# Optimization experiments

Hardware: AMD Instinct MI355X
Metric: run time of the kernel (lower is better)

Reference implementation:

```python
import jax, jax.numpy as jnp
import numpy as np
import math

NUM_HEADS = 8
Q_STRIDE = 2
KV_STRIDE = 2
POS_MAG = 1.0
WAVE_LEN = 1000.0


def _pos_embedding(h, w, h_kv, w_kv, feat_dim):
    # sinusoidal embedding of coordinate differences (in input-resolution units)
    h_idxs = jnp.arange(h, dtype=jnp.float32) * Q_STRIDE
    w_idxs = jnp.arange(w, dtype=jnp.float32) * Q_STRIDE
    h_kv_idxs = jnp.arange(h_kv, dtype=jnp.float32) * KV_STRIDE
    w_kv_idxs = jnp.arange(w_kv, dtype=jnp.float32) * KV_STRIDE
    h_diff = (h_idxs[:, None] - h_kv_idxs[None, :]) * POS_MAG  # [h, h_kv]
    w_diff = (w_idxs[:, None] - w_kv_idxs[None, :]) * POS_MAG  # [w, w_kv]
    feat_range = jnp.arange(feat_dim // 4, dtype=jnp.float32)
    dim_mat = WAVE_LEN ** (4.0 / feat_dim * feat_range)       # [feat_dim/4]
    ang_x = w_diff[:, :, None] / dim_mat                       # [w, w_kv, feat_dim/4]
    ang_y = h_diff[:, :, None] / dim_mat                       # [h, h_kv, feat_dim/4]
    emb_x = jnp.concatenate([jnp.sin(ang_x), jnp.cos(ang_x)], axis=2)  # [w, w_kv, feat_dim/2]
    emb_y = jnp.concatenate([jnp.sin(ang_y), jnp.cos(ang_y)], axis=2)  # [h, h_kv, feat_dim/2]
    return emb_x, emb_y


def setup_inputs() -> dict:
    key = jax.random.key(0)
    ks = jax.random.split(key, 10)
    n, C, H, W = 2, 256, 96, 96
    s = 0.05
    return {
        "x": jax.random.normal(ks[0], (n, C, H, W), jnp.float32),
        "Wq": jax.random.normal(ks[1], (C, C), jnp.float32) * s,
        "Wk": jax.random.normal(ks[2], (C, C), jnp.float32) * s,
        "Wv": jax.random.normal(ks[3], (C, C), jnp.float32) * s,
        "Wx": jax.random.normal(ks[4], (C, C // 2), jnp.float32) * s,
        "Wy": jax.random.normal(ks[5], (C, C // 2), jnp.float32) * s,
        "appr_bias": jax.random.normal(ks[6], (C,), jnp.float32) * s,
        "Wp": jax.random.normal(ks[7], (C, C), jnp.float32) * s,
        "bp": jax.random.normal(ks[8], (C,), jnp.float32) * s,
        "gamma": jax.random.normal(ks[9], (1,), jnp.float32),
    }


def reference(x, Wq, Wk, Wv, Wx, Wy, appr_bias, Wp, bp, gamma):
    n, C, H, W = x.shape
    g = NUM_HEADS
    d = C // g  # qk_embed_dim == v_dim
    # AvgPool2d(kernel_size=1, stride=s) == strided subsampling
    x_q = x[:, :, ::Q_STRIDE, ::Q_STRIDE]
    x_kv = x[:, :, ::KV_STRIDE, ::KV_STRIDE]
    h, w = x_q.shape[2], x_q.shape[3]
    h_kv, w_kv = x_kv.shape[2], x_kv.shape[3]

    # 1x1 convs (no bias) == channel matmuls
    q = jnp.einsum('oc,nchw->nohw', Wq, x_q)   # [n, C, h, w]
    k = jnp.einsum('oc,nchw->nohw', Wk, x_kv)  # [n, C, h_kv, w_kv]
    v = jnp.einsum('oc,nchw->nohw', Wv, x_kv)  # [n, C, h_kv, w_kv]

    emb_x, emb_y = _pos_embedding(h, w, h_kv, w_kv, C)
    inv_sqrt2 = 1.0 / math.sqrt(2.0)
    # Linear(feat_dim/2 -> C), split into heads, scale by 1/sqrt(2)
    pos_x = (jnp.einsum('wvf,of->wvo', emb_x, Wx).reshape(w, w_kv, g, d)
             .transpose(2, 0, 1, 3)) * inv_sqrt2  # [g, w, w_kv, d]
    pos_y = (jnp.einsum('huf,of->huo', emb_y, Wy).reshape(h, h_kv, g, d)
             .transpose(2, 0, 1, 3)) * inv_sqrt2  # [g, h, h_kv, d]

    qr = q.reshape(n, g, d, h, w).transpose(0, 1, 3, 4, 2)  # [n, g, h, w, d]
    kr = k.reshape(n, g, d, h_kv * w_kv)                     # [n, g, d, kv]

    # bias . key term, broadcast over query positions
    e_key = jnp.einsum('gd,ngdk->ngk', appr_bias.reshape(g, d), kr)
    e_key = e_key.reshape(n, g, 1, 1, h_kv, w_kv)
    # query . pos_x term (broadcast over h_kv), query . pos_y term (broadcast over w_kv)
    e_x = jnp.einsum('nghwd,gwvd->nghwv', qr, pos_x)[:, :, :, :, None, :]
    e_y = jnp.einsum('nghwd,ghud->nghwu', qr, pos_y)[:, :, :, :, :, None]

    energy = (e_key + e_x + e_y).reshape(n, g, h * w, h_kv * w_kv)
    attn = jax.nn.softmax(energy, axis=-1)  # [n, g, hw, kv]

    vr = v.reshape(n, g, d, h_kv * w_kv)  # [n, g, d, kv]
    out = jnp.einsum('ngqk,ngdk->ngdq', attn, vr).reshape(n, C, h, w)

    out = jnp.einsum('oc,nchw->nohw', Wp, out) + bp[None, :, None, None]
    out = jax.image.resize(out, (n, C, H, W), method='bilinear')
    return gamma * out + x
```

## Files before the change

kernel.cpp:

```cpp
#include <hip/hip_runtime.h>
#include <hip/hip_bf16.h>
#include <math.h>

#define NB 2
#define CC 256
#define NPOS 2304
#define NDELTA 95

typedef __attribute__((ext_vector_type(8))) short short8;
typedef __attribute__((ext_vector_type(4))) float floatx4;

__device__ inline unsigned short f2bf(float x) {
    unsigned int u = __float_as_uint(x);
    u = (u + 0x7FFFu + ((u >> 16) & 1u)) >> 16;
    return (unsigned short)u;
}
__device__ inline unsigned int pk2(float a, float b) {
    return (unsigned int)f2bf(a) | ((unsigned int)f2bf(b) << 16);
}
__device__ inline unsigned int pkmul(unsigned int a, unsigned int b) {
    __hip_bfloat162 x = *(__hip_bfloat162*)&a;
    __hip_bfloat162 y = *(__hip_bfloat162*)&b;
    __hip_bfloat162 r = __hmul2(x, y);
    return *(unsigned int*)&r;
}

__global__ __launch_bounds__(256) void pos_tables_kernel(
    const float* __restrict__ Wx, const float* __restrict__ Wy,
    const float* __restrict__ Wk, const float* __restrict__ ab,
    unsigned short* __restrict__ posxb, unsigned short* __restrict__ posyb,
    float* __restrict__ wkeff)
{
    int b = blockIdx.x;
    int t = threadIdx.x;
    if (b < NDELTA) {
        __shared__ float emb[128];
        float delta = (float)(b - 47);
        if (t < 64) {
            float dim_inv = exp2f(-(float)t * 0.15571537944784511f);
            float ang = 2.0f * delta * dim_inv;
            emb[t]      = sinf(ang);
            emb[t + 64] = cosf(ang);
        }
        __syncthreads();
        float sx = 0.f, sy = 0.f;
        const float* wxr = Wx + t * 128;
        const float* wyr = Wy + t * 128;
        for (int f = 0; f < 128; ++f) {
            float e = emb[f];
            sx += e * wxr[f];
            sy += e * wyr[f];
        }
        const float inv_sqrt2 = 0.70710678118654752440f;
        int g = t >> 5, d = t & 31;
        posxb[((size_t)g * 96 + b) * 32 + d] = f2bf(sx * inv_sqrt2);
        posyb[((size_t)g * 96 + b) * 32 + d] = f2bf(sy * inv_sqrt2);
    } else if (b < NDELTA + 8) {
        int g = b - NDELTA;
        float s = 0.f;
        for (int d = 0; d < 32; ++d)
            s += ab[g * 32 + d] * Wk[(g * 32 + d) * 256 + t];
        wkeff[g * 256 + t] = s;
    } else {
        int g = t >> 5, d = t & 31;
        posxb[((size_t)g * 96 + 95) * 32 + d] = 0;
        posyb[((size_t)g * 96 + 95) * 32 + d] = 0;
    }
}

__global__ __launch_bounds__(256) void extract_kernel(
    const float* __restrict__ x, float* __restrict__ xs)
{
    int idx = blockIdx.x * 256 + threadIdx.x;
    int f = idx * 4;
    int nc = f / NPOS;
    int rem = f - nc * NPOS;
    int i = rem / 48, j = rem - i * 48;
    const float* row = x + (size_t)nc * (96 * 96) + (2 * i) * 96 + 2 * j;
    *(float4*)(xs + f) = make_float4(row[0], row[2], row[4], row[6]);
}

__global__ __launch_bounds__(256) void wconv_kernel(
    const float* __restrict__ Wq, const float* __restrict__ Wv,
    const float* __restrict__ wkeff, const float* __restrict__ Wp,
    unsigned short* __restrict__ Wb, unsigned short* __restrict__ Wpb)
{
    int o = blockIdx.x;
    int t = threadIdx.x;
    if (o < 576) {
        float v = 0.f;
        if (o < 256)      v = Wq[o * 256 + t];
        else if (o < 512) v = Wv[(o - 256) * 256 + t];
        else if (o < 520) v = wkeff[(o - 512) * 256 + t];
        Wb[(size_t)o * 256 + t] = f2bf(v);
    } else {
        int o2 = o - 576;
        Wpb[(size_t)o2 * 256 + t] = f2bf(Wp[o2 * 256 + t]);
    }
}

__global__ __launch_bounds__(256) void qkv_kernel(
    const float* __restrict__ xs, const unsigned short* __restrict__ Wb,
    unsigned short* __restrict__ qbuf, float* __restrict__ vbuf,
    float* __restrict__ ek)
{
    __shared__ __align__(16) unsigned short Bt[64 * 40];
    int mTile = blockIdx.x;
    int nTile = blockIdx.y;
    int t = threadIdx.x;
    int m = t >> 6, L = t & 63, l16 = L & 15, oct = L >> 4;
    int colBase = nTile * 64;
    int n = colBase / NPOS;
    int p0 = colBase - n * NPOS;
    int o0 = mTile * 64 + m * 16;

    floatx4 acc[4] = {{0,0,0,0},{0,0,0,0},{0,0,0,0},{0,0,0,0}};

    int sc = t >> 4;
    int sp = (t & 15) * 4;
    for (int k0 = 0; k0 < 256; k0 += 32) {
        __syncthreads();
        #pragma unroll
        for (int i = 0; i < 2; ++i) {
            int c = k0 + i * 16 + sc;
            float4 v = *(const float4*)(xs + ((size_t)(n * 256 + c)) * NPOS + p0 + sp);
            int cl = i * 16 + sc;
            Bt[(sp + 0) * 40 + cl] = f2bf(v.x);
            Bt[(sp + 1) * 40 + cl] = f2bf(v.y);
            Bt[(sp + 2) * 40 + cl] = f2bf(v.z);
            Bt[(sp + 3) * 40 + cl] = f2bf(v.w);
        }
        short8 a = *(const short8*)(Wb + (size_t)(o0 + l16) * 256 + k0 + oct * 8);
        __syncthreads();
        #pragma unroll
        for (int f = 0; f < 4; ++f) {
            short8 b = *(const short8*)&Bt[(f * 16 + l16) * 40 + oct * 8];
            acc[f] = __builtin_amdgcn_mfma_f32_16x16x32_bf16(a, b, acc[f], 0, 0, 0);
        }
    }

    #pragma unroll
    for (int f = 0; f < 4; ++f) {
        int p = p0 + f * 16 + l16;
        #pragma unroll
        for (int r = 0; r < 4; ++r) {
            int o = o0 + oct * 4 + r;
            float val = acc[f][r];
            if (o < 256) {
                int g = o >> 5, d = o & 31;
                qbuf[((size_t)(n * 8 + g) * NPOS + p) * 32 + d] = f2bf(val);
            } else if (o < 512) {
                vbuf[((size_t)(n * 256 + (o - 256))) * NPOS + p] = val;
            } else if (o < 520) {
                ek[((size_t)(n * 8 + (o - 512))) * NPOS + p] = val;
            }
        }
    }
}

__global__ __launch_bounds__(256) void softA_kernel(float* __restrict__ ekA)
{
    int ng = blockIdx.x;
    float* e = ekA + (size_t)ng * NPOS;
    int t = threadIdx.x;
    __shared__ float red[256];
    float m = -1e30f;
    for (int k = t; k < NPOS; k += 256) m = fmaxf(m, e[k]);
    red[t] = m;
    __syncthreads();
    for (int s = 128; s > 0; s >>= 1) {
        if (t < s) red[t] = fmaxf(red[t], red[t + s]);
        __syncthreads();
    }
    m = red[0];
    for (int k = t; k < NPOS; k += 256) e[k] = __expf(e[k] - m);
}

__global__ __launch_bounds__(256) void vhat_kernel(
    const float* __restrict__ vbuf, const float* __restrict__ ekA,
    uint4* __restrict__ vhat)
{
    int tile = blockIdx.x;
    int ng = blockIdx.y;
    int k0 = tile * 96;
    int t = threadIdx.x;
    const float* vb = vbuf + (size_t)ng * 32 * NPOS;
    const float* Ab = ekA + (size_t)ng * NPOS;
    uint4* out = vhat + ((size_t)ng * 24 + tile) * 576;

    for (int s = t; s < 576; s += 256) {
        int grp = s >> 6;
        int Ls = s & 63;
        int cc = grp / 3;
        int nn = grp - cc * 3;
        int koct = cc * 32 + ((Ls >> 4) << 3);
        uint4 w = make_uint4(0u, 0u, 0u, 0u);
        if (nn < 2) {
            int d = nn * 16 + (Ls & 15);
            const float* vp = vb + (size_t)d * NPOS + k0 + koct;
            const float* ap = Ab + k0 + koct;
            float4 v0 = *(const float4*)vp;
            float4 v1 = *(const float4*)(vp + 4);
            float4 a0 = *(const float4*)ap;
            float4 a1 = *(const float4*)(ap + 4);
            w.x = pk2(v0.x * a0.x, v0.y * a0.y);
            w.y = pk2(v0.z * a0.z, v0.w * a0.w);
            w.z = pk2(v1.x * a1.x, v1.y * a1.y);
            w.w = pk2(v1.z * a1.z, v1.w * a1.w);
        } else if ((Ls & 15) == 0) {
            const float* ap = Ab + k0 + koct;
            float4 a0 = *(const float4*)ap;
            float4 a1 = *(const float4*)(ap + 4);
            w.x = pk2(a0.x, a0.y);
            w.y = pk2(a0.z, a0.w);
            w.z = pk2(a1.x, a1.y);
            w.w = pk2(a1.z, a1.w);
        }
        out[s] = w;
    }
}

#define DO_TILE(BB, TT) do {                                                   \
    int u0_ = (TT) * 2;                                                        \
    unsigned int y0_ = Ys[qp * 50 + u0_];     y0_ |= y0_ << 16;                \
    unsigned int y1_ = Ys[qp * 50 + u0_ + 1]; y1_ |= y1_ << 16;                \
    unsigned int Yc0_ = y0_, Yc1_ = (o < 2) ? y0_ : y1_, Yc2_ = y1_;           \
    union { unsigned int u[4]; short8 s; } av_;                                \
    av_.u[0] = pkmul(Xp[0], Yc0_); av_.u[1] = pkmul(Xp[1], Yc0_);              \
    av_.u[2] = pkmul(Xp[2], Yc0_); av_.u[3] = pkmul(Xp[3], Yc0_);              \
    acc0 = __builtin_amdgcn_mfma_f32_16x16x32_bf16(av_.s, *(const short8*)&BB[0], acc0, 0, 0, 0); \
    acc1 = __builtin_amdgcn_mfma_f32_16x16x32_bf16(av_.s, *(const short8*)&BB[1], acc1, 0, 0, 0); \
    acc2 = __builtin_amdgcn_mfma_f32_16x16x32_bf16(av_.s, *(const short8*)&BB[2], acc2, 0, 0, 0); \
    av_.u[0] = pkmul(Xp[4], Yc1_); av_.u[1] = pkmul(Xp[5], Yc1_);              \
    av_.u[2] = pkmul(Xp[6], Yc1_); av_.u[3] = pkmul(Xp[7], Yc1_);              \
    acc0 = __builtin_amdgcn_mfma_f32_16x16x32_bf16(av_.s, *(const short8*)&BB[3], acc0, 0, 0, 0); \
    acc1 = __builtin_amdgcn_mfma_f32_16x16x32_bf16(av_.s, *(const short8*)&BB[4], acc1, 0, 0, 0); \
    acc2 = __builtin_amdgcn_mfma_f32_16x16x32_bf16(av_.s, *(const short8*)&BB[5], acc2, 0, 0, 0); \
    av_.u[0] = pkmul(Xp[8], Yc2_); av_.u[1] = pkmul(Xp[9], Yc2_);              \
    av_.u[2] = pkmul(Xp[10], Yc2_); av_.u[3] = pkmul(Xp[11], Yc2_);            \
    acc0 = __builtin_amdgcn_mfma_f32_16x16x32_bf16(av_.s, *(const short8*)&BB[6], acc0, 0, 0, 0); \
    acc1 = __builtin_amdgcn_mfma_f32_16x16x32_bf16(av_.s, *(const short8*)&BB[7], acc1, 0, 0, 0); \
    acc2 = __builtin_amdgcn_mfma_f32_16x16x32_bf16(av_.s, *(const short8*)&BB[8], acc2, 0, 0, 0); \
} while (0)

__global__ __launch_bounds__(256, 2) void attn_kernel(
    const unsigned short* __restrict__ qbuf, const unsigned short* __restrict__ posxb,
    const unsigned short* __restrict__ posyb, const uint4* __restrict__ vhat,
    float* __restrict__ oattn)
{
    __shared__ unsigned short Xs[64 * 50];
    __shared__ unsigned short Ys[64 * 50];
    __shared__ float linv_s[64];

    int blk = blockIdx.x;
    int qt = blk % 36;
    int ng = blk / 36;
    int nb = ng >> 3, g = ng & 7;
    int qbase = qt * 64;
    int t = threadIdx.x;
    int m = t >> 6, L = t & 63;
    int l16 = L & 15, oct = L >> 4;

    {
        int qtile0 = qbase + m * 16;
        int hq = qtile0 / 48;
        int wq0 = qtile0 - hq * 48;
        short8 aq = *(const short8*)(qbuf +
            ((size_t)ng * NPOS + qtile0 + l16) * 32 + oct * 8);
        const unsigned short* pxg = posxb + (size_t)g * 96 * 32;
        const unsigned short* pyg = posyb + (size_t)g * 96 * 32;
        floatx4 zero = {0.f, 0.f, 0.f, 0.f};
        #pragma unroll
        for (int j = 0; j < 6; ++j) {
            int dl = j * 16 + l16;
            short8 bx = *(const short8*)(pxg + (size_t)dl * 32 + oct * 8);
            short8 by = *(const short8*)(pyg + (size_t)dl * 32 + oct * 8);
            floatx4 tx = __builtin_amdgcn_mfma_f32_16x16x32_bf16(aq, bx, zero, 0, 0, 0);
            floatx4 ty = __builtin_amdgcn_mfma_f32_16x16x32_bf16(aq, by, zero, 0, 0, 0);
            int u = hq + 47 - dl;
            bool uok = (u >= 0) && (u < 48);
            #pragma unroll
            for (int r = 0; r < 4; ++r) {
                int ql = oct * 4 + r;
                int v = wq0 + ql + 47 - dl;
                if (v >= 0 && v < 48)
                    Xs[(m * 16 + ql) * 50 + v] = f2bf(__expf(tx[r]));
                if (uok)
                    Ys[(m * 16 + ql) * 50 + u] = f2bf(__expf(ty[r]));
            }
        }
    }
    __syncthreads();

    int qp = m * 16 + l16;
    int o = oct;
    unsigned int Xp[12];
    #pragma unroll
    for (int c = 0; c < 3; ++c)
        #pragma unroll
        for (int jj = 0; jj < 4; ++jj) {
            int k = c * 32 + o * 8 + jj * 2;
            int v0 = (k < 48) ? k : k - 48;
            Xp[c * 4 + jj] = *(const unsigned int*)&Xs[qp * 50 + v0];
        }

    floatx4 acc0 = {0.f, 0.f, 0.f, 0.f};
    floatx4 acc1 = {0.f, 0.f, 0.f, 0.f};
    floatx4 acc2 = {0.f, 0.f, 0.f, 0.f};

    const uint4* vb = vhat + (size_t)ng * 24 * 576 + L;
    uint4 Abuf[9], Bbuf[9];
    #pragma unroll
    for (int gg = 0; gg < 9; ++gg) Abuf[gg] = vb[gg * 64];

    for (int tile = 0; tile < 24; tile += 2) {
        const uint4* sB = vb + (tile + 1) * 576;
        #pragma unroll
        for (int gg = 0; gg < 9; ++gg) Bbuf[gg] = sB[gg * 64];
        DO_TILE(Abuf, tile);
        if (tile + 2 < 24) {
            const uint4* sA = vb + (tile + 2) * 576;
            #pragma unroll
            for (int gg = 0; gg < 9; ++gg) Abuf[gg] = sA[gg * 64];
        }
        DO_TILE(Bbuf, tile + 1);
    }

    if ((L & 15) == 0) {
        int qc = m * 16 + (L >> 4) * 4;
        #pragma unroll
        for (int r = 0; r < 4; ++r)
            linv_s[qc + r] = 1.0f / acc2[r];
    }
    __syncthreads();
    {
        int qc = m * 16 + (L >> 4) * 4;
        float4 li = *(const float4*)&linv_s[qc];
        int d0 = L & 15;
        float* r0 = oattn + ((size_t)(nb * 256 + g * 32 + d0)) * NPOS + qbase + qc;
        *(float4*)r0 = make_float4(acc0[0] * li.x, acc0[1] * li.y,
                                   acc0[2] * li.z, acc0[3] * li.w);
        float* r1 = oattn + ((size_t)(nb * 256 + g * 32 + 16 + d0)) * NPOS + qbase + qc;
        *(float4*)r1 = make_float4(acc1[0] * li.x, acc1[1] * li.y,
                                   acc1[2] * li.z, acc1[3] * li.w);
    }
}

__global__ __launch_bounds__(256) void proj_kernel(
    const float* __restrict__ oattn, const unsigned short* __restrict__ Wpb,
    const float* __restrict__ bpv, float* __restrict__ proj)
{
    __shared__ __align__(16) unsigned short Bt[64 * 40];
    int mTile = blockIdx.x;
    int nTile = blockIdx.y;
    int t = threadIdx.x;
    int m = t >> 6, L = t & 63, l16 = L & 15, oct = L >> 4;
    int colBase = nTile * 64;
    int n = colBase / NPOS;
    int p0 = colBase - n * NPOS;
    int o0 = mTile * 64 + m * 16;

    floatx4 acc[4] = {{0,0,0,0},{0,0,0,0},{0,0,0,0},{0,0,0,0}};

    int sc = t >> 4;
    int sp = (t & 15) * 4;
    for (int k0 = 0; k0 < 256; k0 += 32) {
        __syncthreads();
        #pragma unroll
        for (int i = 0; i < 2; ++i) {
            int c = k0 + i * 16 + sc;
            float4 v = *(const float4*)(oattn + ((size_t)(n * 256 + c)) * NPOS + p0 + sp);
            int cl = i * 16 + sc;
            Bt[(sp + 0) * 40 + cl] = f2bf(v.x);
            Bt[(sp + 1) * 40 + cl] = f2bf(v.y);
            Bt[(sp + 2) * 40 + cl] = f2bf(v.z);
            Bt[(sp + 3) * 40 + cl] = f2bf(v.w);
        }
        short8 a = *(const short8*)(Wpb + (size_t)(o0 + l16) * 256 + k0 + oct * 8);
        __syncthreads();
        #pragma unroll
        for (int f = 0; f < 4; ++f) {
            short8 b = *(const short8*)&Bt[(f * 16 + l16) * 40 + oct * 8];
            acc[f] = __builtin_amdgcn_mfma_f32_16x16x32_bf16(a, b, acc[f], 0, 0, 0);
        }
    }

    #pragma unroll
    for (int f = 0; f < 4; ++f) {
        int p = p0 + f * 16 + l16;
        #pragma unroll
        for (int r = 0; r < 4; ++r) {
            int o = o0 + oct * 4 + r;
            proj[((size_t)(n * 256 + o)) * NPOS + p] = acc[f][r] + bpv[o];
        }
    }
}

__global__ __launch_bounds__(256) void resize_kernel(
    const float* __restrict__ proj, const float* __restrict__ x,
    const float* __restrict__ gamma, float* __restrict__ out)
{
    int idx = blockIdx.x * 256 + threadIdx.x;
    int J = idx % 96;
    int tmp = idx / 96;
    int I = tmp % 96;
    int nc = tmp / 96;

    int jr = I >> 1;
    int r0, r1; float w0, w1;
    if ((I & 1) == 0) { r0 = (jr > 0) ? jr - 1 : 0; r1 = jr; w0 = 0.25f; w1 = 0.75f; }
    else              { r0 = jr; r1 = (jr < 47) ? jr + 1 : 47; w0 = 0.75f; w1 = 0.25f; }
    int jc = J >> 1;
    int c0, c1; float u0, u1;
    if ((J & 1) == 0) { c0 = (jc > 0) ? jc - 1 : 0; c1 = jc; u0 = 0.25f; u1 = 0.75f; }
    else              { c0 = jc; c1 = (jc < 47) ? jc + 1 : 47; u0 = 0.75f; u1 = 0.25f; }

    const float* P = proj + (size_t)nc * NPOS;
    float v = w0 * (u0 * P[r0 * 48 + c0] + u1 * P[r0 * 48 + c1]) +
              w1 * (u0 * P[r1 * 48 + c0] + u1 * P[r1 * 48 + c1]);
    out[idx] = gamma[0] * v + x[idx];
}

extern "C" void kernel_launch(void* const* d_in, const int* in_sizes, int n_in,
                              void* d_out, int out_size, void* d_ws, size_t ws_size,
                              hipStream_t stream)
{
    const float* x     = (const float*)d_in[0];
    const float* Wq    = (const float*)d_in[1];
    const float* Wk    = (const float*)d_in[2];
    const float* Wv    = (const float*)d_in[3];
    const float* Wx    = (const float*)d_in[4];
    const float* Wy    = (const float*)d_in[5];
    const float* ab    = (const float*)d_in[6];
    const float* Wp    = (const float*)d_in[7];
    const float* bp    = (const float*)d_in[8];
    const float* gamma = (const float*)d_in[9];
    float* out = (float*)d_out;

    unsigned short* posxb = (unsigned short*)d_ws;
    unsigned short* posyb = posxb + 8 * 96 * 32;
    float* wkeff = (float*)(posyb + 8 * 96 * 32);
    unsigned short* Wb  = (unsigned short*)(wkeff + 8 * 256);
    unsigned short* Wpb = Wb + (size_t)576 * 256;
    unsigned short* qbuf = Wpb + (size_t)256 * 256;
    float* vbuf  = (float*)(qbuf + (size_t)2 * 8 * NPOS * 32);
    float* ekA   = vbuf + (size_t)2 * 8 * NPOS * 32;
    float* oattn = ekA + 2 * 8 * NPOS;
    float* proj  = oattn + (size_t)2 * 256 * NPOS;
    float* xs    = oattn;
    uint4* vhat  = (uint4*)proj;

    hipLaunchKernelGGL(pos_tables_kernel, dim3(104), dim3(256), 0, stream,
                       Wx, Wy, Wk, ab, posxb, posyb, wkeff);
    hipLaunchKernelGGL(extract_kernel, dim3(1152), dim3(256), 0, stream, x, xs);
    hipLaunchKernelGGL(wconv_kernel, dim3(832), dim3(256), 0, stream,
                       Wq, Wv, wkeff, Wp, Wb, Wpb);
    hipLaunchKernelGGL(qkv_kernel, dim3(9, 72), dim3(256), 0, stream,
                       xs, Wb, qbuf, vbuf, ekA);
    hipLaunchKernelGGL(softA_kernel, dim3(16), dim3(256), 0, stream, ekA);
    hipLaunchKernelGGL(vhat_kernel, dim3(24, 16), dim3(256), 0, stream,
                       vbuf, ekA, vhat);
    hipLaunchKernelGGL(attn_kernel, dim3(576), dim3(256), 0, stream,
                       qbuf, posxb, posyb, vhat, oattn);
    hipLaunchKernelGGL(proj_kernel, dim3(4, 72), dim3(256), 0, stream,
                       oattn, Wpb, bp, proj);
    hipLaunchKernelGGL(resize_kernel, dim3((2 * 256 * 96 * 96) / 256), dim3(256), 0, stream,
                       proj, x, gamma, out);
}
```

Before: 171.2 us.

## Store GEMM operands as transposed bf16 and drop LDS staging in projections

New measurement: 168.6 us. Within noise of the previous version (-1.6%).

```diff
diff --git a/kernel.cpp b/kernel.cpp
--- a/kernel.cpp
+++ b/kernel.cpp
@@ -14,6 +14,9 @@
     unsigned int u = __float_as_uint(x);
     u = (u + 0x7FFFu + ((u >> 16) & 1u)) >> 16;
     return (unsigned short)u;
+}
+__device__ inline float bf2f(unsigned short h) {
+    return __uint_as_float(((unsigned int)h) << 16);
 }
 __device__ inline unsigned int pk2(float a, float b) {
     return (unsigned int)f2bf(a) | ((unsigned int)f2bf(b) << 16);
@@ -25,11 +28,13 @@
     return *(unsigned int*)&r;
 }
 
-__global__ __launch_bounds__(256) void pos_tables_kernel(
+__global__ __launch_bounds__(256) void prep_kernel(
     const float* __restrict__ Wx, const float* __restrict__ Wy,
     const float* __restrict__ Wk, const float* __restrict__ ab,
+    const float* __restrict__ Wq, const float* __restrict__ Wv,
+    const float* __restrict__ Wp,
     unsigned short* __restrict__ posxb, unsigned short* __restrict__ posyb,
-    float* __restrict__ wkeff)
+    unsigned short* __restrict__ Wb, unsigned short* __restrict__ Wpb)
 {
     int b = blockIdx.x;
     int t = threadIdx.x;
@@ -55,104 +60,116 @@
         int g = t >> 5, d = t & 31;
         posxb[((size_t)g * 96 + b) * 32 + d] = f2bf(sx * inv_sqrt2);
         posyb[((size_t)g * 96 + b) * 32 + d] = f2bf(sy * inv_sqrt2);
-    } else if (b < NDELTA + 8) {
-        int g = b - NDELTA;
-        float s = 0.f;
-        for (int d = 0; d < 32; ++d)
-            s += ab[g * 32 + d] * Wk[(g * 32 + d) * 256 + t];
-        wkeff[g * 256 + t] = s;
-    } else {
+    } else if (b == NDELTA) {
         int g = t >> 5, d = t & 31;
         posxb[((size_t)g * 96 + 95) * 32 + d] = 0;
         posyb[((size_t)g * 96 + 95) * 32 + d] = 0;
-    }
-}
-
-__global__ __launch_bounds__(256) void extract_kernel(
-    const float* __restrict__ x, float* __restrict__ xs)
-{
-    int idx = blockIdx.x * 256 + threadIdx.x;
-    int f = idx * 4;
-    int nc = f / NPOS;
-    int rem = f - nc * NPOS;
-    int i = rem / 48, j = rem - i * 48;
-    const float* row = x + (size_t)nc * (96 * 96) + (2 * i) * 96 + 2 * j;
-    *(float4*)(xs + f) = make_float4(row[0], row[2], row[4], row[6]);
-}
-
-__global__ __launch_bounds__(256) void wconv_kernel(
-    const float* __restrict__ Wq, const float* __restrict__ Wv,
-    const float* __restrict__ wkeff, const float* __restrict__ Wp,
-    unsigned short* __restrict__ Wb, unsigned short* __restrict__ Wpb)
-{
-    int o = blockIdx.x;
-    int t = threadIdx.x;
-    if (o < 576) {
+    } else if (b < 96 + 640) {
+        int o = b - 96;
         float v = 0.f;
         if (o < 256)      v = Wq[o * 256 + t];
         else if (o < 512) v = Wv[(o - 256) * 256 + t];
-        else if (o < 520) v = wkeff[(o - 512) * 256 + t];
+        else if (o < 520) {
+            int g = o - 512;
+            float s = 0.f;
+            for (int d = 0; d < 32; ++d)
+                s += ab[g * 32 + d] * Wk[(g * 32 + d) * 256 + t];
+            v = s;
+        }
         Wb[(size_t)o * 256 + t] = f2bf(v);
     } else {
-        int o2 = o - 576;
-        Wpb[(size_t)o2 * 256 + t] = f2bf(Wp[o2 * 256 + t]);
-    }
-}
-
-__global__ __launch_bounds__(256) void qkv_kernel(
-    const float* __restrict__ xs, const unsigned short* __restrict__ Wb,
+        int o = b - 736;
+        Wpb[(size_t)o * 256 + t] = f2bf(Wp[o * 256 + t]);
+    }
+}
+
+__global__ __launch_bounds__(256) void extract_kernel(
+    const float* __restrict__ x, unsigned short* __restrict__ xs_t)
+{
+    __shared__ __align__(16) unsigned short Lt[64][264];
+    int blk = blockIdx.x;
+    int pt = blk % 36;
+    int n = blk / 36;
+    int p0 = pt * 64;
+    int t = threadIdx.x;
+    int cw = t >> 4;
+    int pl = t & 15;
+
+    for (int cc = 0; cc < 16; ++cc) {
+        int c = cc * 16 + cw;
+        const float* src = x + ((size_t)(n * 256 + c)) * (96 * 96);
+        #pragma unroll
+        for (int k = 0; k < 4; ++k) {
+            int p = p0 + pl + k * 16;
+            int i = p / 48, j = p - i * 48;
+            Lt[pl + k * 16][c] = f2bf(src[(2 * i) * 96 + 2 * j]);
+        }
+    }
+    __syncthreads();
+    #pragma unroll
+    for (int it = 0; it < 8; ++it) {
+        int s = t + it * 256;
+        int p = s >> 5, c8 = s & 31;
+        uint4 v = *(const uint4*)&Lt[p][c8 * 8];
+        *(uint4*)(xs_t + ((size_t)(n * NPOS + p0 + p)) * 256 + c8 * 8) = v;
+    }
+}
+
+__global__ __launch_bounds__(256, 2) void qkv_kernel(
+    const unsigned short* __restrict__ xs_t, const unsigned short* __restrict__ Wb,
     unsigned short* __restrict__ qbuf, float* __restrict__ vbuf,
     float* __restrict__ ek)
 {
-    __shared__ __align__(16) unsigned short Bt[64 * 40];
-    int mTile = blockIdx.x;
-    int nTile = blockIdx.y;
-    int t = threadIdx.x;
-    int m = t >> 6, L = t & 63, l16 = L & 15, oct = L >> 4;
-    int colBase = nTile * 64;
+    int mT = blockIdx.x;
+    int nT = blockIdx.y;
+    int t = threadIdx.x;
+    int wm = t >> 6, L = t & 63, l16 = L & 15, oct = L >> 4;
+    int colBase = nT * 64;
     int n = colBase / NPOS;
     int p0 = colBase - n * NPOS;
-    int o0 = mTile * 64 + m * 16;
-
-    floatx4 acc[4] = {{0,0,0,0},{0,0,0,0},{0,0,0,0},{0,0,0,0}};
-
-    int sc = t >> 4;
-    int sp = (t & 15) * 4;
-    for (int k0 = 0; k0 < 256; k0 += 32) {
-        __syncthreads();
-        #pragma unroll
-        for (int i = 0; i < 2; ++i) {
-            int c = k0 + i * 16 + sc;
-            float4 v = *(const float4*)(xs + ((size_t)(n * 256 + c)) * NPOS + p0 + sp);
-            int cl = i * 16 + sc;
-            Bt[(sp + 0) * 40 + cl] = f2bf(v.x);
-            Bt[(sp + 1) * 40 + cl] = f2bf(v.y);
-            Bt[(sp + 2) * 40 + cl] = f2bf(v.z);
-            Bt[(sp + 3) * 40 + cl] = f2bf(v.w);
-        }
-        short8 a = *(const short8*)(Wb + (size_t)(o0 + l16) * 256 + k0 + oct * 8);
-        __syncthreads();
+    int o_w = mT * 128 + wm * 32;
+
+    const unsigned short* A0 = Wb + (size_t)(o_w + l16) * 256 + oct * 8;
+    const unsigned short* A1 = A0 + 16 * 256;
+    const unsigned short* B0 = xs_t + ((size_t)(n * NPOS + p0 + l16)) * 256 + oct * 8;
+
+    floatx4 acc[2][4] = {};
+    #pragma unroll
+    for (int kc = 0; kc < 8; ++kc) {
+        int k0 = kc * 32;
+        short8 a0 = *(const short8*)(A0 + k0);
+        short8 a1 = *(const short8*)(A1 + k0);
+        short8 b0 = *(const short8*)(B0 + k0);
+        short8 b1 = *(const short8*)(B0 + 16 * 256 + k0);
+        short8 b2 = *(const short8*)(B0 + 32 * 256 + k0);
+        short8 b3 = *(const short8*)(B0 + 48 * 256 + k0);
+        acc[0][0] = __builtin_amdgcn_mfma_f32_16x16x32_bf16(a0, b0, acc[0][0], 0, 0, 0);
+        acc[0][1] = __builtin_amdgcn_mfma_f32_16x16x32_bf16(a0, b1, acc[0][1], 0, 0, 0);
+        acc[0][2] = __builtin_amdgcn_mfma_f32_16x16x32_bf16(a0, b2, acc[0][2], 0, 0, 0);
+        acc[0][3] = __builtin_amdgcn_mfma_f32_16x16x32_bf16(a0, b3, acc[0][3], 0, 0, 0);
+        acc[1][0] = __builtin_amdgcn_mfma_f32_16x16x32_bf16(a1, b0, acc[1][0], 0, 0, 0);
+        acc[1][1] = __builtin_amdgcn_mfma_f32_16x16x32_bf16(a1, b1, acc[1][1], 0, 0, 0);
+        acc[1][2] = __builtin_amdgcn_mfma_f32_16x16x32_bf16(a1, b2, acc[1][2], 0, 0, 0);
+        acc[1][3] = __builtin_amdgcn_mfma_f32_16x16x32_bf16(a1, b3, acc[1][3], 0, 0, 0);
+    }
+
+    #pragma unroll
+    for (int af = 0; af < 2; ++af) {
         #pragma unroll
         for (int f = 0; f < 4; ++f) {
-            short8 b = *(const short8*)&Bt[(f * 16 + l16) * 40 + oct * 8];
-            acc[f] = __builtin_amdgcn_mfma_f32_16x16x32_bf16(a, b, acc[f], 0, 0, 0);
-        }
-    }
-
-    #pragma unroll
-    for (int f = 0; f < 4; ++f) {
-        int p = p0 + f * 16 + l16;
-        #pragma unroll
-        for (int r = 0; r < 4; ++r) {
-            int o = o0 + oct * 4 + r;
-            float val = acc[f][r];
-            if (o < 256) {
-                int g = o >> 5, d = o & 31;
-                qbuf[((size_t)(n * 8 + g) * NPOS + p) * 32 + d] = f2bf(val);
-            } else if (o < 512) {
-                vbuf[((size_t)(n * 256 + (o - 256))) * NPOS + p] = val;
-            } else if (o < 520) {
-                ek[((size_t)(n * 8 + (o - 512))) * NPOS + p] = val;
+            int p = p0 + f * 16 + l16;
+            #pragma unroll
+            for (int r = 0; r < 4; ++r) {
+                int o = o_w + af * 16 + oct * 4 + r;
+                float val = acc[af][f][r];
+                if (o < 256) {
+                    int g = o >> 5, d = o & 31;
+                    qbuf[((size_t)(n * 8 + g) * NPOS + p) * 32 + d] = f2bf(val);
+                } else if (o < 512) {
+                    vbuf[((size_t)(n * 256 + (o - 256))) * NPOS + p] = val;
+                } else if (o < 520) {
+                    ek[((size_t)(n * 8 + (o - 512))) * NPOS + p] = val;
+                }
             }
         }
     }
@@ -246,7 +263,7 @@
 __global__ __launch_bounds__(256, 2) void attn_kernel(
     const unsigned short* __restrict__ qbuf, const unsigned short* __restrict__ posxb,
     const unsigned short* __restrict__ posyb, const uint4* __restrict__ vhat,
-    float* __restrict__ oattn)
+    unsigned short* __restrict__ oattn_t)
 {
     __shared__ unsigned short Xs[64 * 50];
     __shared__ unsigned short Ys[64 * 50];
@@ -335,69 +352,70 @@
     __syncthreads();
     {
         int qc = m * 16 + (L >> 4) * 4;
-        float4 li = *(const float4*)&linv_s[qc];
         int d0 = L & 15;
-        float* r0 = oattn + ((size_t)(nb * 256 + g * 32 + d0)) * NPOS + qbase + qc;
-        *(float4*)r0 = make_float4(acc0[0] * li.x, acc0[1] * li.y,
-                                   acc0[2] * li.z, acc0[3] * li.w);
-        float* r1 = oattn + ((size_t)(nb * 256 + g * 32 + 16 + d0)) * NPOS + qbase + qc;
-        *(float4*)r1 = make_float4(acc1[0] * li.x, acc1[1] * li.y,
-                                   acc1[2] * li.z, acc1[3] * li.w);
-    }
-}
-
-__global__ __launch_bounds__(256) void proj_kernel(
-    const float* __restrict__ oattn, const unsigned short* __restrict__ Wpb,
-    const float* __restrict__ bpv, float* __restrict__ proj)
-{
-    __shared__ __align__(16) unsigned short Bt[64 * 40];
-    int mTile = blockIdx.x;
-    int nTile = blockIdx.y;
-    int t = threadIdx.x;
-    int m = t >> 6, L = t & 63, l16 = L & 15, oct = L >> 4;
-    int colBase = nTile * 64;
+        #pragma unroll
+        for (int r = 0; r < 4; ++r) {
+            float lir = linv_s[qc + r];
+            size_t row = ((size_t)nb * NPOS + qbase + qc + r) * 256;
+            oattn_t[row + g * 32 + d0]      = f2bf(acc0[r] * lir);
+            oattn_t[row + g * 32 + 16 + d0] = f2bf(acc1[r] * lir);
+        }
+    }
+}
+
+__global__ __launch_bounds__(256, 2) void proj_kernel(
+    const unsigned short* __restrict__ oattn_t, const unsigned short* __restrict__ Wpb,
+    const float* __restrict__ bpv, unsigned short* __restrict__ projb)
+{
+    int mT = blockIdx.x;
+    int nT = blockIdx.y;
+    int t = threadIdx.x;
+    int wm = t >> 6, L = t & 63, l16 = L & 15, oct = L >> 4;
+    int colBase = nT * 64;
     int n = colBase / NPOS;
     int p0 = colBase - n * NPOS;
-    int o0 = mTile * 64 + m * 16;
-
-    floatx4 acc[4] = {{0,0,0,0},{0,0,0,0},{0,0,0,0},{0,0,0,0}};
-
-    int sc = t >> 4;
-    int sp = (t & 15) * 4;
-    for (int k0 = 0; k0 < 256; k0 += 32) {
-        __syncthreads();
-        #pragma unroll
-        for (int i = 0; i < 2; ++i) {
-            int c = k0 + i * 16 + sc;
-            float4 v = *(const float4*)(oattn + ((size_t)(n * 256 + c)) * NPOS + p0 + sp);
-            int cl = i * 16 + sc;
-            Bt[(sp + 0) * 40 + cl] = f2bf(v.x);
-            Bt[(sp + 1) * 40 + cl] = f2bf(v.y);
-            Bt[(sp + 2) * 40 + cl] = f2bf(v.z);
-            Bt[(sp + 3) * 40 + cl] = f2bf(v.w);
-        }
-        short8 a = *(const short8*)(Wpb + (size_t)(o0 + l16) * 256 + k0 + oct * 8);
-        __syncthreads();
+    int o_w = mT * 128 + wm * 32;
+
+    const unsigned short* A0 = Wpb + (size_t)(o_w + l16) * 256 + oct * 8;
+    const unsigned short* A1 = A0 + 16 * 256;
+    const unsigned short* B0 = oattn_t + ((size_t)(n * NPOS + p0 + l16)) * 256 + oct * 8;
+
+    floatx4 acc[2][4] = {};
+    #pragma unroll
+    for (int kc = 0; kc < 8; ++kc) {
+        int k0 = kc * 32;
+        short8 a0 = *(const short8*)(A0 + k0);
+        short8 a1 = *(const short8*)(A1 + k0);
+        short8 b0 = *(const short8*)(B0 + k0);
+        short8 b1 = *(const short8*)(B0 + 16 * 256 + k0);
+        short8 b2 = *(const short8*)(B0 + 32 * 256 + k0);
+        short8 b3 = *(const short8*)(B0 + 48 * 256 + k0);
+        acc[0][0] = __builtin_amdgcn_mfma_f32_16x16x32_bf16(a0, b0, acc[0][0], 0, 0, 0);
+        acc[0][1] = __builtin_amdgcn_mfma_f32_16x16x32_bf16(a0, b1, acc[0][1], 0, 0, 0);
+        acc[0][2] = __builtin_amdgcn_mfma_f32_16x16x32_bf16(a0, b2, acc[0][2], 0, 0, 0);
+        acc[0][3] = __builtin_amdgcn_mfma_f32_16x16x32_bf16(a0, b3, acc[0][3], 0, 0, 0);
+        acc[1][0] = __builtin_amdgcn_mfma_f32_16x16x32_bf16(a1, b0, acc[1][0], 0, 0, 0);
+        acc[1][1] = __builtin_amdgcn_mfma_f32_16x16x32_bf16(a1, b1, acc[1][1], 0, 0, 0);
+        acc[1][2] = __builtin_amdgcn_mfma_f32_16x16x32_bf16(a1, b2, acc[1][2], 0, 0, 0);
+        acc[1][3] = __builtin_amdgcn_mfma_f32_16x16x32_bf16(a1, b3, acc[1][3], 0, 0, 0);
+    }
+
+    #pragma unroll
+    for (int af = 0; af < 2; ++af) {
         #pragma unroll
         for (int f = 0; f < 4; ++f) {
-            short8 b = *(const short8*)&Bt[(f * 16 + l16) * 40 + oct * 8];
-            acc[f] = __builtin_amdgcn_mfma_f32_16x16x32_bf16(a, b, acc[f], 0, 0, 0);
-        }
-    }
-
-    #pragma unroll
-    for (int f = 0; f < 4; ++f) {
-        int p = p0 + f * 16 + l16;
-        #pragma unroll
-        for (int r = 0; r < 4; ++r) {
-            int o = o0 + oct * 4 + r;
-            proj[((size_t)(n * 256 + o)) * NPOS + p] = acc[f][r] + bpv[o];
+            int p = p0 + f * 16 + l16;
+            #pragma unroll
+            for (int r = 0; r < 4; ++r) {
+                int o = o_w + af * 16 + oct * 4 + r;
+                projb[((size_t)(n * 256 + o)) * NPOS + p] = f2bf(acc[af][f][r] + bpv[o]);
+            }
         }
     }
 }
 
 __global__ __launch_bounds__(256) void resize_kernel(
-    const float* __restrict__ proj, const float* __restrict__ x,
+    const unsigned short* __restrict__ projb, const float* __restrict__ x,
     const float* __restrict__ gamma, float* __restrict__ out)
 {
     int idx = blockIdx.x * 256 + threadIdx.x;
@@ -415,9 +433,9 @@
     if ((J & 1) == 0) { c0 = (jc > 0) ? jc - 1 : 0; c1 = jc; u0 = 0.25f; u1 = 0.75f; }
     else              { c0 = jc; c1 = (jc < 47) ? jc + 1 : 47; u0 = 0.75f; u1 = 0.25f; }
 
-    const float* P = proj + (size_t)nc * NPOS;
-    float v = w0 * (u0 * P[r0 * 48 + c0] + u1 * P[r0 * 48 + c1]) +
-              w1 * (u0 * P[r1 * 48 + c0] + u1 * P[r1 * 48 + c1]);
+    const unsigned short* P = projb + (size_t)nc * NPOS;
+    float v = w0 * (u0 * bf2f(P[r0 * 48 + c0]) + u1 * bf2f(P[r0 * 48 + c1])) +
+              w1 * (u0 * bf2f(P[r1 * 48 + c0]) + u1 * bf2f(P[r1 * 48 + c1]));
     out[idx] = gamma[0] * v + x[idx];
 }
 
@@ -438,32 +456,29 @@
     float* out = (float*)d_out;
 
     unsigned short* posxb = (unsigned short*)d_ws;
-    unsigned short* posyb = posxb + 8 * 96 * 32;
-    float* wkeff = (float*)(posyb + 8 * 96 * 32);
-    unsigned short* Wb  = (unsigned short*)(wkeff + 8 * 256);
-    unsigned short* Wpb = Wb + (size_t)576 * 256;
-    unsigned short* qbuf = Wpb + (size_t)256 * 256;
-    float* vbuf  = (float*)(qbuf + (size_t)2 * 8 * NPOS * 32);
-    float* ekA   = vbuf + (size_t)2 * 8 * NPOS * 32;
-    float* oattn = ekA + 2 * 8 * NPOS;
-    float* proj  = oattn + (size_t)2 * 256 * NPOS;
-    float* xs    = oattn;
-    uint4* vhat  = (uint4*)proj;
-
-    hipLaunchKernelGGL(pos_tables_kernel, dim3(104), dim3(256), 0, stream,
-                       Wx, Wy, Wk, ab, posxb, posyb, wkeff);
-    hipLaunchKernelGGL(extract_kernel, dim3(1152), dim3(256), 0, stream, x, xs);
-    hipLaunchKernelGGL(wconv_kernel, dim3(832), dim3(256), 0, stream,
-                       Wq, Wv, wkeff, Wp, Wb, Wpb);
-    hipLaunchKernelGGL(qkv_kernel, dim3(9, 72), dim3(256), 0, stream,
-                       xs, Wb, qbuf, vbuf, ekA);
+    unsigned short* posyb  = posxb + 8 * 96 * 32;
+    unsigned short* Wb     = posyb + 8 * 96 * 32;
+    unsigned short* Wpb    = Wb + (size_t)640 * 256;
+    unsigned short* xs_t   = Wpb + (size_t)256 * 256;
+    unsigned short* qbuf   = xs_t + (size_t)2 * NPOS * 256;
+    unsigned short* oattn_t= qbuf + (size_t)2 * NPOS * 256;
+    unsigned short* projb  = oattn_t + (size_t)2 * NPOS * 256;
+    float* vbuf  = (float*)(projb + (size_t)2 * NPOS * 256);
+    float* ekA   = vbuf + (size_t)2 * 256 * NPOS;
+    uint4* vhat  = (uint4*)(ekA + 16 * NPOS);
+
+    hipLaunchKernelGGL(prep_kernel, dim3(992), dim3(256), 0, stream,
+                       Wx, Wy, Wk, ab, Wq, Wv, Wp, posxb, posyb, Wb, Wpb);
+    hipLaunchKernelGGL(extract_kernel, dim3(72), dim3(256), 0, stream, x, xs_t);
+    hipLaunchKernelGGL(qkv_kernel, dim3(5, 72), dim3(256), 0, stream,
+                       xs_t, Wb, qbuf, vbuf, ekA);
     hipLaunchKernelGGL(softA_kernel, dim3(16), dim3(256), 0, stream, ekA);
     hipLaunchKernelGGL(vhat_kernel, dim3(24, 16), dim3(256), 0, stream,
                        vbuf, ekA, vhat);
     hipLaunchKernelGGL(attn_kernel, dim3(576), dim3(256), 0, stream,
-                       qbuf, posxb, posyb, vhat, oattn);
-    hipLaunchKernelGGL(proj_kernel, dim3(4, 72), dim3(256), 0, stream,
-                       oattn, Wpb, bp, proj);
+                       qbuf, posxb, posyb, vhat, oattn_t);
+    hipLaunchKernelGGL(proj_kernel, dim3(2, 72), dim3(256), 0, stream,
+                       oattn_t, Wpb, bp, projb);
     hipLaunchKernelGGL(resize_kernel, dim3((2 * 256 * 96 * 96) / 256), dim3(256), 0, stream,
-                       proj, x, gamma, out);
-}
+                       projb, x, gamma, out);
+}
```
